# Kernel optimization log

Measured on AMD Instinct MI355X. Metric: run time of the kernel, lower is better.

The kernel has to match this reference:

```python
import jax, jax.numpy as jnp
import numpy as np

B_, N, C, NH, NW = 4096, 64, 128, 4, 2048
HD = C // NH
SCALE = HD ** -0.5


def setup_inputs() -> dict:
    key = jax.random.key(0)
    ks = jax.random.split(key, 6)
    x = jax.random.normal(ks[0], (B_, N, C), jnp.float32)
    y = jax.random.normal(ks[1], (B_, N, C), jnp.float32)
    P_thermal = jax.random.normal(ks[2], (B_, NH, N, N), jnp.float32)
    mask = jax.random.normal(ks[3], (NW, N, N), jnp.float32)
    qkv_w = jax.random.normal(ks[4], (2 * C, C), jnp.float32) * (C ** -0.5)
    qkv_b = jnp.zeros((2 * C,), jnp.float32)
    proj_w = jax.random.normal(ks[5], (C, C), jnp.float32) * (C ** -0.5)
    proj_b = jnp.zeros((C,), jnp.float32)
    lambda_ = jnp.float32(1.0)
    return {"x": x, "y": y, "P_thermal": P_thermal, "mask": mask,
            "qkv_w": qkv_w, "qkv_b": qkv_b, "proj_w": proj_w,
            "proj_b": proj_b, "lambda_": lambda_}


def reference(x, y, P_thermal, mask, qkv_w, qkv_b, proj_w, proj_b, lambda_):
    # q: raw reshape of x (faithful to the original: no projection, axis-mixing reshape)
    q = x.reshape(B_, NH, N, HD) * SCALE                    # [B_, H, N, hd]
    # kv projection: dim -> 2*dim, then split into k, v
    kv = (y @ qkv_w.T + qkv_b).reshape(B_, N, 2, NH, HD).transpose(2, 0, 3, 1, 4)
    k, v = kv[0], kv[1]                                     # [B_, H, N, hd]
    attn = jnp.einsum('bhnd,bhmd->bhnm', q, k)              # [B_, H, N, N]
    # shift-window additive mask: [nW, N, N] broadcast over (batch, heads)
    attn = (attn.reshape(B_ // NW, NW, NH, N, N) + mask[None, :, None]).reshape(B_, NH, N, N)
    # learnable thermal bias
    attn = attn + lambda_ * P_thermal
    attn = jax.nn.softmax(attn, axis=-1)
    out = jnp.einsum('bhnm,bhmd->bhnd', attn, v)            # [B_, H, N, hd]
    out = out.transpose(0, 2, 1, 3).reshape(B_, N, C)       # [B_, N, C]
    return out @ proj_w.T + proj_b
```

## Files before the change

### kernel.cpp

```cpp
#include <hip/hip_runtime.h>


typedef unsigned short u16;
typedef __attribute__((ext_vector_type(8))) __bf16 bf16x8;
typedef __attribute__((ext_vector_type(4))) float f32x4;
typedef __attribute__((ext_vector_type(8))) float f32x8;

#define SCALE 0.17677669529663687f

__device__ __forceinline__ float b2f(u16 u) {
  union { float f; unsigned i; } x; x.i = ((unsigned)u) << 16; return x.f;
}
__device__ __forceinline__ u16 f2b(float f) {
  unsigned u = __float_as_uint(f);
  u = u + 0x7FFFu + ((u >> 16) & 1u);
  return (u16)(u >> 16);
}
__device__ __forceinline__ bf16x8 ldb16(const u16* p) {
  bf16x8 v; __builtin_memcpy(&v, (const void*)p, 16); return v;
}
__device__ __forceinline__ bf16x8 ldb8x2(const u16* p) {
  bf16x8 v; __builtin_memcpy(&v, (const void*)p, 8);
  __builtin_memcpy((char*)&v + 8, (const void*)(p + 4), 8); return v;
}
__device__ __forceinline__ f32x8 ldf8(const float* p) {
  f32x8 v; __builtin_memcpy(&v, (const void*)p, 32); return v;
}
__device__ __forceinline__ void split8(const f32x8 f, bf16x8* h, bf16x8* l) {
#pragma unroll
  for (int j = 0; j < 8; ++j) {
    float fj = f[j];
    __bf16 hj = (__bf16)fj;
    (*h)[j] = hj;
    (*l)[j] = (__bf16)(fj - (float)hj);
  }
}


__global__ __launch_bounds__(256, 3) void wattn(
    const float* __restrict__ x, const float* __restrict__ y,
    const float* __restrict__ P, const float* __restrict__ msk,
    const float* __restrict__ qkvw, const float* __restrict__ qkvb,
    const float* __restrict__ projw, const float* __restrict__ projb,
    const float* __restrict__ lamp, float* __restrict__ out)
{
  __shared__ u16 sm[26624];
  u16* v_s = sm;
  u16* k_s = sm + 9216;
  u16* p_s = sm + 9216;
  u16* o_s = sm;

  const int b    = blockIdx.x;
  const int tid  = threadIdx.x;
  const int w    = tid >> 6;
  const int lane = tid & 63;
  const int q    = lane >> 4;
  const int r    = lane & 15;
  const float lam = lamp[0];
  const f32x4 zf = {0.f, 0.f, 0.f, 0.f};

  {
    const float* yb = y + (size_t)b * 8192;
#pragma unroll
    for (int hf = 0; hf < 2; ++hf) {
      bf16x8 bwh[2][4], bwl[2][4];
      float bias[2];
#pragma unroll
      for (int c2 = 0; c2 < 2; ++c2) {
        int col = (w * 4 + hf * 2 + c2) * 16 + r;
        bias[c2] = qkvb[col];
#pragma unroll
        for (int ks = 0; ks < 4; ++ks) {
          f32x8 bw = ldf8(qkvw + col * 128 + ks * 32 + q * 8);
          split8(bw, &bwh[c2][ks], &bwl[c2][ks]);
        }
      }
#pragma unroll
      for (int nt = 0; nt < 4; ++nt) {
        bf16x8 ayh[4], ayl[4];
#pragma unroll
        for (int ks = 0; ks < 4; ++ks) {
          f32x8 ay = ldf8(yb + (nt * 16 + r) * 128 + ks * 32 + q * 8);
          split8(ay, &ayh[ks], &ayl[ks]);
        }
#pragma unroll
        for (int c2 = 0; c2 < 2; ++c2) {
          f32x4 acc = zf;
#pragma unroll
          for (int ks = 0; ks < 4; ++ks) {
            acc = __builtin_amdgcn_mfma_f32_16x16x32_bf16(ayh[ks], bwh[c2][ks], acc, 0, 0, 0);
            acc = __builtin_amdgcn_mfma_f32_16x16x32_bf16(ayh[ks], bwl[c2][ks], acc, 0, 0, 0);
            acc = __builtin_amdgcn_mfma_f32_16x16x32_bf16(ayl[ks], bwh[c2][ks], acc, 0, 0, 0);
          }
          int col = (w * 4 + hf * 2 + c2) * 16 + r;
#pragma unroll
          for (int i = 0; i < 4; ++i) {
            float val = acc[i] + bias[c2];
            int n = nt * 16 + q * 4 + i;
            if (w < 2) {
              int h_ = col >> 5, d = col & 31;
              k_s[(h_ * 64 + n) * 40 + d] = f2b(val);
            } else {
              int c3 = col - 128;
              int h_ = c3 >> 5, d = c3 & 31;
              v_s[(h_ * 32 + d) * 72 + n] = f2b(val);
            }
          }
        }
      }
    }
  }
  __syncthreads();

  f32x4 s[4][4];
  {
    const float* xq = x + (size_t)b * 8192 + w * 2048;
    bf16x8 aqh[4], aql[4], bk[4];
#pragma unroll
    for (int nt = 0; nt < 4; ++nt) {
      f32x8 a = ldf8(xq + (nt * 16 + r) * 32 + q * 8);
      split8(a, &aqh[nt], &aql[nt]);
    }
#pragma unroll
    for (int mt = 0; mt < 4; ++mt)
      bk[mt] = ldb16(k_s + (w * 64 + mt * 16 + r) * 40 + q * 8);
#pragma unroll
    for (int nt = 0; nt < 4; ++nt)
#pragma unroll
      for (int mt = 0; mt < 4; ++mt) {
        f32x4 t = __builtin_amdgcn_mfma_f32_16x16x32_bf16(aqh[nt], bk[mt], zf, 0, 0, 0);
        s[nt][mt] = __builtin_amdgcn_mfma_f32_16x16x32_bf16(aql[nt], bk[mt], t, 0, 0, 0);
      }
  }
  __syncthreads();
  {
    const float* Pb = P + ((size_t)b * 4 + w) * 4096;
    const float* mb = msk + (size_t)(b & 2047) * 4096;
#pragma unroll
    for (int nt = 0; nt < 4; ++nt) {
#pragma unroll
      for (int i = 0; i < 4; ++i) {
        int n = nt * 16 + q * 4 + i;
        float sv[4];
#pragma unroll
        for (int mt = 0; mt < 4; ++mt) {
          int m = mt * 16 + r;
          sv[mt] = s[nt][mt][i] * SCALE + mb[n * 64 + m] + lam * Pb[n * 64 + m];
        }
        float mx = fmaxf(fmaxf(sv[0], sv[1]), fmaxf(sv[2], sv[3]));
        mx = fmaxf(mx, __shfl_xor(mx, 1));
        mx = fmaxf(mx, __shfl_xor(mx, 2));
        mx = fmaxf(mx, __shfl_xor(mx, 4));
        mx = fmaxf(mx, __shfl_xor(mx, 8));
        float e[4], sum = 0.f;
#pragma unroll
        for (int mt = 0; mt < 4; ++mt) { e[mt] = __expf(sv[mt] - mx); sum += e[mt]; }
        sum += __shfl_xor(sum, 1);
        sum += __shfl_xor(sum, 2);
        sum += __shfl_xor(sum, 4);
        sum += __shfl_xor(sum, 8);
        float inv = 1.0f / sum;
#pragma unroll
        for (int mt = 0; mt < 4; ++mt)
          p_s[(w * 64 + n) * 68 + mt * 16 + r] = f2b(e[mt] * inv);
      }
    }
  }
  __syncthreads();

  f32x4 o[4][2];
  {
    bf16x8 bv[2][2];
#pragma unroll
    for (int dt = 0; dt < 2; ++dt)
#pragma unroll
      for (int ks = 0; ks < 2; ++ks)
        bv[dt][ks] = ldb16(v_s + (w * 32 + dt * 16 + r) * 72 + ks * 32 + q * 8);
#pragma unroll
    for (int nt = 0; nt < 4; ++nt) {
      bf16x8 ap[2];
#pragma unroll
      for (int ks = 0; ks < 2; ++ks)
        ap[ks] = ldb8x2(p_s + (w * 64 + nt * 16 + r) * 68 + ks * 32 + q * 8);
#pragma unroll
      for (int dt = 0; dt < 2; ++dt) {
        f32x4 t = zf;
        t = __builtin_amdgcn_mfma_f32_16x16x32_bf16(ap[0], bv[dt][0], t, 0, 0, 0);
        t = __builtin_amdgcn_mfma_f32_16x16x32_bf16(ap[1], bv[dt][1], t, 0, 0, 0);
        o[nt][dt] = t;
      }
    }
  }
  __syncthreads();
#pragma unroll
  for (int nt = 0; nt < 4; ++nt)
#pragma unroll
    for (int dt = 0; dt < 2; ++dt)
#pragma unroll
      for (int i = 0; i < 4; ++i)
        o_s[(nt * 16 + q * 4 + i) * 136 + w * 32 + dt * 16 + r] = f2b(o[nt][dt][i]);
  __syncthreads();

  {
    bf16x8 bph[2][4], bpl[2][4];
    float bias2[2];
#pragma unroll
    for (int c2 = 0; c2 < 2; ++c2) {
      int col = (w * 2 + c2) * 16 + r;
      bias2[c2] = projb[col];
#pragma unroll
      for (int ks = 0; ks < 4; ++ks) {
        f32x8 bp = ldf8(projw + col * 128 + ks * 32 + q * 8);
        split8(bp, &bph[c2][ks], &bpl[c2][ks]);
      }
    }
    float* ob = out + (size_t)b * 8192;
#pragma unroll
    for (int nt = 0; nt < 4; ++nt) {
      bf16x8 ao[4];
#pragma unroll
      for (int ks = 0; ks < 4; ++ks)
        ao[ks] = ldb16(o_s + (nt * 16 + r) * 136 + ks * 32 + q * 8);
#pragma unroll
      for (int c2 = 0; c2 < 2; ++c2) {
        f32x4 acc = zf;
#pragma unroll
        for (int ks = 0; ks < 4; ++ks) {
          acc = __builtin_amdgcn_mfma_f32_16x16x32_bf16(ao[ks], bph[c2][ks], acc, 0, 0, 0);
          acc = __builtin_amdgcn_mfma_f32_16x16x32_bf16(ao[ks], bpl[c2][ks], acc, 0, 0, 0);
        }
        int col = (w * 2 + c2) * 16 + r;
#pragma unroll
        for (int i = 0; i < 4; ++i)
          ob[(nt * 16 + q * 4 + i) * 128 + col] = acc[i] + bias2[c2];
      }
    }
  }
}

extern "C" void kernel_launch(void* const* d_in, const int* in_sizes, int n_in,
                              void* d_out, int out_size, void* d_ws, size_t ws_size,
                              hipStream_t stream) {
  (void)in_sizes; (void)n_in; (void)out_size; (void)d_ws; (void)ws_size;
  wattn<<<dim3(4096), dim3(256), 0, stream>>>(
      (const float*)d_in[0],
      (const float*)d_in[1],
      (const float*)d_in[2],
      (const float*)d_in[3],
      (const float*)d_in[4],
      (const float*)d_in[5],
      (const float*)d_in[6],
      (const float*)d_in[7],
      (const float*)d_in[8],
      (float*)d_out);
}
```

Before: 734.6 us.

## Transpose QK^T MFMA, prefetch x/P/mask/proj weights, and fuse softmax per tile

Loads x early, before the KV projection. P and mask tiles are double-buffered in registers so they are fetched one row tile ahead of the scores that need them. QK^T now uses K as the A operand, so each lane holds 4 contiguous columns of one row; this allows 16-byte vectorised loads of P and mask, a cross-lane reduction of only 2 shuffles, and packed 8-byte bf16 stores of probabilities into LDS. The projection weights are loaded before the LDS barrier to hide their latency. In exchange, register pressure rises from the buffered P/mask/x/weight values, which may hurt occupancy at the 3-blocks launch bound.

```diff
diff --git a/kernel.cpp b/kernel.cpp
--- a/kernel.cpp
+++ b/kernel.cpp
@@ -3,14 +3,12 @@
 
 typedef unsigned short u16;
 typedef __attribute__((ext_vector_type(8))) __bf16 bf16x8;
+typedef __attribute__((ext_vector_type(4))) __bf16 bf16x4;
 typedef __attribute__((ext_vector_type(4))) float f32x4;
 typedef __attribute__((ext_vector_type(8))) float f32x8;
 
 #define SCALE 0.17677669529663687f
 
-__device__ __forceinline__ float b2f(u16 u) {
-  union { float f; unsigned i; } x; x.i = ((unsigned)u) << 16; return x.f;
-}
 __device__ __forceinline__ u16 f2b(float f) {
   unsigned u = __float_as_uint(f);
   u = u + 0x7FFFu + ((u >> 16) & 1u);
@@ -25,6 +23,9 @@
 }
 __device__ __forceinline__ f32x8 ldf8(const float* p) {
   f32x8 v; __builtin_memcpy(&v, (const void*)p, 32); return v;
+}
+__device__ __forceinline__ f32x4 ldf4(const float* p) {
+  f32x4 v; __builtin_memcpy(&v, (const void*)p, 16); return v;
 }
 __device__ __forceinline__ void split8(const f32x8 f, bf16x8* h, bf16x8* l) {
 #pragma unroll
@@ -59,6 +60,22 @@
   const float lam = lamp[0];
   const f32x4 zf = {0.f, 0.f, 0.f, 0.f};
 
+  const float* xq = x + (size_t)b * 8192 + w * 2048;
+  f32x8 xr[4];
+#pragma unroll
+  for (int nt = 0; nt < 4; ++nt)
+    xr[nt] = ldf8(xq + (nt * 16 + r) * 32 + q * 8);
+
+  const float* Pb = P + ((size_t)b * 4 + w) * 4096;
+  const float* mb = msk + (size_t)(b & 2047) * 4096;
+  f32x4 bP[2][4], bM[2][4];
+#pragma unroll
+  for (int mt = 0; mt < 4; ++mt) {
+    int off = r * 64 + mt * 16 + q * 4;
+    bP[0][mt] = ldf4(Pb + off);
+    bM[0][mt] = ldf4(mb + off);
+  }
+
   {
     const float* yb = y + (size_t)b * 8192;
 #pragma unroll
@@ -112,57 +129,56 @@
   }
   __syncthreads();
 
-  f32x4 s[4][4];
-  {
-    const float* xq = x + (size_t)b * 8192 + w * 2048;
-    bf16x8 aqh[4], aql[4], bk[4];
-#pragma unroll
-    for (int nt = 0; nt < 4; ++nt) {
-      f32x8 a = ldf8(xq + (nt * 16 + r) * 32 + q * 8);
-      split8(a, &aqh[nt], &aql[nt]);
-    }
+  {
+    bf16x8 bk[4];
 #pragma unroll
     for (int mt = 0; mt < 4; ++mt)
       bk[mt] = ldb16(k_s + (w * 64 + mt * 16 + r) * 40 + q * 8);
-#pragma unroll
-    for (int nt = 0; nt < 4; ++nt)
+    __syncthreads();
+
+#pragma unroll
+    for (int nt = 0; nt < 4; ++nt) {
+      if (nt < 3) {
+#pragma unroll
+        for (int mt = 0; mt < 4; ++mt) {
+          int off = ((nt + 1) * 16 + r) * 64 + mt * 16 + q * 4;
+          bP[(nt + 1) & 1][mt] = ldf4(Pb + off);
+          bM[(nt + 1) & 1][mt] = ldf4(mb + off);
+        }
+      }
+      bf16x8 ah, al;
+      split8(xr[nt], &ah, &al);
+      f32x4 sv4[4];
 #pragma unroll
       for (int mt = 0; mt < 4; ++mt) {
-        f32x4 t = __builtin_amdgcn_mfma_f32_16x16x32_bf16(aqh[nt], bk[mt], zf, 0, 0, 0);
-        s[nt][mt] = __builtin_amdgcn_mfma_f32_16x16x32_bf16(aql[nt], bk[mt], t, 0, 0, 0);
-      }
-  }
-  __syncthreads();
-  {
-    const float* Pb = P + ((size_t)b * 4 + w) * 4096;
-    const float* mb = msk + (size_t)(b & 2047) * 4096;
-#pragma unroll
-    for (int nt = 0; nt < 4; ++nt) {
-#pragma unroll
-      for (int i = 0; i < 4; ++i) {
-        int n = nt * 16 + q * 4 + i;
-        float sv[4];
-#pragma unroll
-        for (int mt = 0; mt < 4; ++mt) {
-          int m = mt * 16 + r;
-          sv[mt] = s[nt][mt][i] * SCALE + mb[n * 64 + m] + lam * Pb[n * 64 + m];
-        }
-        float mx = fmaxf(fmaxf(sv[0], sv[1]), fmaxf(sv[2], sv[3]));
-        mx = fmaxf(mx, __shfl_xor(mx, 1));
-        mx = fmaxf(mx, __shfl_xor(mx, 2));
-        mx = fmaxf(mx, __shfl_xor(mx, 4));
-        mx = fmaxf(mx, __shfl_xor(mx, 8));
-        float e[4], sum = 0.f;
-#pragma unroll
-        for (int mt = 0; mt < 4; ++mt) { e[mt] = __expf(sv[mt] - mx); sum += e[mt]; }
-        sum += __shfl_xor(sum, 1);
-        sum += __shfl_xor(sum, 2);
-        sum += __shfl_xor(sum, 4);
-        sum += __shfl_xor(sum, 8);
-        float inv = 1.0f / sum;
-#pragma unroll
-        for (int mt = 0; mt < 4; ++mt)
-          p_s[(w * 64 + n) * 68 + mt * 16 + r] = f2b(e[mt] * inv);
+        f32x4 t = __builtin_amdgcn_mfma_f32_16x16x32_bf16(bk[mt], ah, zf, 0, 0, 0);
+        t = __builtin_amdgcn_mfma_f32_16x16x32_bf16(bk[mt], al, t, 0, 0, 0);
+        sv4[mt] = t * SCALE + bM[nt & 1][mt] + lam * bP[nt & 1][mt];
+      }
+      f32x4 m4 = sv4[0];
+#pragma unroll
+      for (int mt = 1; mt < 4; ++mt)
+#pragma unroll
+        for (int i = 0; i < 4; ++i) m4[i] = fmaxf(m4[i], sv4[mt][i]);
+      float mx = fmaxf(fmaxf(m4[0], m4[1]), fmaxf(m4[2], m4[3]));
+      mx = fmaxf(mx, __shfl_xor(mx, 16));
+      mx = fmaxf(mx, __shfl_xor(mx, 32));
+      f32x4 e4[4];
+#pragma unroll
+      for (int mt = 0; mt < 4; ++mt)
+#pragma unroll
+        for (int i = 0; i < 4; ++i) e4[mt][i] = __expf(sv4[mt][i] - mx);
+      f32x4 t4 = e4[0] + e4[1] + e4[2] + e4[3];
+      float sum = (t4[0] + t4[1]) + (t4[2] + t4[3]);
+      sum += __shfl_xor(sum, 16);
+      sum += __shfl_xor(sum, 32);
+      float inv = 1.0f / sum;
+#pragma unroll
+      for (int mt = 0; mt < 4; ++mt) {
+        bf16x4 pk;
+#pragma unroll
+        for (int i = 0; i < 4; ++i) pk[i] = (__bf16)(e4[mt][i] * inv);
+        __builtin_memcpy(p_s + (w * 64 + nt * 16 + r) * 68 + mt * 16 + q * 4, &pk, 8);
       }
     }
   }
@@ -191,6 +207,18 @@
       }
     }
   }
+
+  f32x8 bpr[2][4];
+  float bias2[2];
+#pragma unroll
+  for (int c2 = 0; c2 < 2; ++c2) {
+    int col = (w * 2 + c2) * 16 + r;
+    bias2[c2] = projb[col];
+#pragma unroll
+    for (int ks = 0; ks < 4; ++ks)
+      bpr[c2][ks] = ldf8(projw + col * 128 + ks * 32 + q * 8);
+  }
+
   __syncthreads();
 #pragma unroll
   for (int nt = 0; nt < 4; ++nt)
@@ -203,17 +231,11 @@
 
   {
     bf16x8 bph[2][4], bpl[2][4];
-    float bias2[2];
-#pragma unroll
-    for (int c2 = 0; c2 < 2; ++c2) {
-      int col = (w * 2 + c2) * 16 + r;
-      bias2[c2] = projb[col];
-#pragma unroll
-      for (int ks = 0; ks < 4; ++ks) {
-        f32x8 bp = ldf8(projw + col * 128 + ks * 32 + q * 8);
-        split8(bp, &bph[c2][ks], &bpl[c2][ks]);
-      }
-    }
+#pragma unroll
+    for (int c2 = 0; c2 < 2; ++c2)
+#pragma unroll
+      for (int ks = 0; ks < 4; ++ks)
+        split8(bpr[c2][ks], &bph[c2][ks], &bpl[c2][ks]);
     float* ob = out + (size_t)b * 8192;
 #pragma unroll
     for (int nt = 0; nt < 4; ++nt) {
```

Result: slower. 838.4 us (+14.1%).
